# Optimization experiments

Measured on AMD Instinct MI355X. Metric: run time of the kernel, lower is better.

## Reference

```python
import jax, jax.numpy as jnp
import numpy as np

VOCAB = 50257
WORD_DIM = 300
HIDDEN = 256
BATCH = 256   # number of trees
LEAVES = 1024  # leaves per complete binary tree (power of 2)


def setup_inputs() -> dict:
    key = jax.random.key(0)
    k_ids, k_emb, k_w1, k_b1, k_w2, k_b2 = jax.random.split(key, 6)
    word_ids = jax.random.randint(k_ids, (BATCH, LEAVES), 0, VOCAB)
    emb_table = jax.random.normal(k_emb, (VOCAB, WORD_DIM), dtype=jnp.float32) * 0.1
    W1 = jax.random.normal(k_w1, (WORD_DIM, HIDDEN), dtype=jnp.float32) * (1.0 / np.sqrt(WORD_DIM))
    b1 = jax.random.normal(k_b1, (HIDDEN,), dtype=jnp.float32) * 0.01
    W2 = jax.random.normal(k_w2, (2 * HIDDEN, HIDDEN), dtype=jnp.float32) * (1.0 / np.sqrt(2 * HIDDEN))
    b2 = jax.random.normal(k_b2, (HIDDEN,), dtype=jnp.float32) * 0.01
    return {"word_ids": word_ids, "emb_table": emb_table, "W1": W1, "b1": b1, "W2": W2, "b2": b2}


def reference(word_ids, emb_table, W1, b1, W2, b2):
    # Leaves: embedding lookup + word2hidden linear (no nonlinearity, as in source)
    h = jnp.einsum('blw,wh->blh', emb_table[word_ids], W1) + b1  # [B, L, H]
    # Internal nodes: concat(left, right) @ W2 + b2, level by level up the
    # complete binary tree. Loop count = log2(LEAVES), a small static constant.
    while h.shape[1] > 1:
        B, n, H = h.shape
        pairs = h.reshape(B, n // 2, 2 * H)  # concat of sibling states
        h = jnp.einsum('bnk,kh->bnh', pairs, W2) + b2
    return h[:, 0, :]  # root hidden state per tree: [B, H]
```

## Files before the change

### kernel.cpp

```cpp
#include <hip/hip_runtime.h>
#include <hip/hip_bf16.h>
#include <stdint.h>

#define VOCAB 50257
#define WD 300
#define KP1 320
#define MP 50432

using bf16 = __hip_bfloat16;
typedef __attribute__((ext_vector_type(4))) float f32x4;
typedef __attribute__((ext_vector_type(8))) short bf16x8;

__device__ __forceinline__ void async_load16(const void* g, void* l) {
    __builtin_amdgcn_global_load_lds(
        (const __attribute__((address_space(1))) uint32_t*)(uintptr_t)g,
        (__attribute__((address_space(3))) uint32_t*)l, 16, 0, 0);
}

__global__ void prep_w(const float* __restrict__ W1, const float* __restrict__ W2,
                       const float* __restrict__ b2,
                       bf16* __restrict__ w1t, bf16* __restrict__ w2t,
                       bf16* __restrict__ w2b, float* __restrict__ b4,
                       float* __restrict__ zbuf) {
    if (blockIdx.x == 1344) {
        __shared__ float b2s[256];
        int n = threadIdx.x;
        b2s[n] = b2[n];
        zbuf[n] = 0.0f;
        __syncthreads();
        float acc = b2s[n];
        #pragma unroll 8
        for (int k = 0; k < 256; ++k)
            acc += b2s[k] * (W2[k * 256 + n] + W2[(k + 256) * 256 + n]);
        b4[n] = acc;
        return;
    }
    int idx = blockIdx.x * 256 + threadIdx.x;
    if (idx < 256 * KP1) {
        int n = idx / KP1;
        int k = idx - n * KP1;
        w1t[idx] = __float2bfloat16(k < WD ? W1[k * 256 + n] : 0.0f);
    } else if (idx < 256 * KP1 + 131072) {
        int j = idx - 256 * KP1;
        int n = j >> 9, k = j & 511;
        w2t[j] = __float2bfloat16(W2[k * 256 + n]);
    } else {
        int j = idx - 256 * KP1 - 131072;
        w2b[j] = __float2bfloat16(W2[j]);
    }
}

template <int AMODE, bool OUT_F32>
__device__ __forceinline__ void tile_gemm(
    char* smem, const void* Av, const int* ids,
    const bf16* BT, int Bstr, const float* bias,
    void* C, int Cs, int coff, int K, int As, int m0,
    const float* zbuf)
{
    constexpr int ASZ = (AMODE == 2) ? 16384 : 8192;
    constexpr int BSZ = 16384, STAGE = ASZ + BSZ;

    const int t = threadIdx.x, w = t >> 6, lane = t & 63;
    const int rg = w >> 2, cgr = w & 3, mi = lane & 15, q = lane >> 4;
    const bf16* Ab = (const bf16*)Av;

    int4 idq = {0, 0, 0, 0};
    if constexpr (AMODE == 1) idq = ((const int4*)ids)[m0 + (t >> 2)];

    auto stage = [&](int ke, int buf) {
        char* Asm = smem + buf * STAGE;
        char* Bsm = Asm + ASZ;
        if constexpr (AMODE == 2) {
            const float* A32 = (const float*)Av;
            #pragma unroll
            for (int i = 0; i < 2; ++i) {
                int s = i * 512 + t;
                int row = s >> 3;
                int kcd = (s & 7) ^ (row & 7);
                int k = ke + kcd * 4;
                int grow = m0 + row; if (grow >= VOCAB) grow = VOCAB - 1;
                const float* g = (k <= 296) ? (A32 + (size_t)grow * WD + k) : zbuf;
                async_load16(g, Asm + i * 8192 + w * 1024);
            }
        } else {
            int row = t >> 2;
            int kcd = (t & 3) ^ ((row >> 2) & 3);
            const bf16* g;
            if constexpr (AMODE == 1) {
                int sel = ke >> 8;
                int id = (sel & 2) ? ((sel & 1) ? idq.w : idq.z)
                                   : ((sel & 1) ? idq.y : idq.x);
                g = Ab + (size_t)id * 256 + (ke & 255) + kcd * 8;
            } else {
                g = Ab + (size_t)(m0 + row) * As + ke + kcd * 8;
            }
            async_load16(g, Asm + w * 1024);
        }
        #pragma unroll
        for (int i = 0; i < 2; ++i) {
            int s = i * 512 + t;
            int col = s >> 2;
            int kcd = (s & 3) ^ ((col >> 2) & 3);
            async_load16(BT + (size_t)col * Bstr + ke + kcd * 8,
                         Bsm + i * 8192 + w * 1024);
        }
    };

    f32x4 acc[4][4] = {};

    auto compute = [&](int buf) {
        const char* Asm = smem + buf * STAGE;
        const bf16* Bs16 = (const bf16*)(Asm + ASZ);
        bf16x8 af[4], bfr[4];
        if constexpr (AMODE == 2) {
            const float* As32 = (const float*)Asm;
            #pragma unroll
            for (int r = 0; r < 4; ++r) {
                int row = rg * 64 + r * 16 + mi;
                int sl = row * 8 + ((2 * q) ^ (row & 7));
                f32x4 lo = *(const f32x4*)(As32 + sl * 4);
                f32x4 hi = *(const f32x4*)(As32 + (sl ^ 1) * 4);
                union { bf16x8 v; bf16 hh[8]; } u;
                #pragma unroll
                for (int j = 0; j < 4; ++j) u.hh[j] = __float2bfloat16(lo[j]);
                #pragma unroll
                for (int j = 0; j < 4; ++j) u.hh[4 + j] = __float2bfloat16(hi[j]);
                af[r] = u.v;
            }
        } else {
            const bf16* As16 = (const bf16*)Asm;
            #pragma unroll
            for (int r = 0; r < 4; ++r) {
                int row = rg * 64 + r * 16 + mi;
                int slot = row * 4 + (q ^ ((row >> 2) & 3));
                af[r] = *(const bf16x8*)(As16 + slot * 8);
            }
        }
        #pragma unroll
        for (int c = 0; c < 4; ++c) {
            int col = cgr * 64 + c * 16 + mi;
            int slot = col * 4 + (q ^ ((col >> 2) & 3));
            bfr[c] = *(const bf16x8*)(Bs16 + slot * 8);
        }
        #pragma unroll
        for (int r = 0; r < 4; ++r)
            #pragma unroll
            for (int c = 0; c < 4; ++c)
                acc[r][c] = __builtin_amdgcn_mfma_f32_16x16x32_bf16(af[r], bfr[c], acc[r][c], 0, 0, 0);
    };

    const int S = K >> 5;
    if constexpr (AMODE == 2) {
        stage(0, 0);
        for (int k0 = 0; k0 < S; ++k0) {
            if (k0 + 1 < S) {
                stage((k0 + 1) * 32, (k0 + 1) & 1);
                asm volatile("s_waitcnt vmcnt(4)\n\ts_barrier" ::: "memory");
            } else {
                asm volatile("s_waitcnt vmcnt(0)\n\ts_barrier" ::: "memory");
            }
            compute(k0 & 1);
            asm volatile("s_waitcnt lgkmcnt(0)\n\ts_barrier" ::: "memory");
        }
    } else {
        stage(0, 0);
        if (S > 1) stage(32, 1);
        for (int k0 = 0; k0 < S; ++k0) {
            if (k0 + 1 < S)
                asm volatile("s_waitcnt vmcnt(3)\n\ts_barrier" ::: "memory");
            else
                asm volatile("s_waitcnt vmcnt(0)\n\ts_barrier" ::: "memory");
            if (k0 + 2 < S) stage((k0 + 2) * 32, (k0 + 2) % 3);
            compute(k0 % 3);
        }
    }

    #pragma unroll
    for (int r = 0; r < 4; ++r) {
        int rowb = m0 + rg * 64 + r * 16 + q * 4;
        #pragma unroll
        for (int c = 0; c < 4; ++c) {
            int col = cgr * 64 + c * 16 + mi;
            float bv = bias[col];
            #pragma unroll
            for (int i = 0; i < 4; ++i) {
                float v = acc[r][c][i] + bv;
                size_t o = (size_t)(rowb + i) * Cs + coff + col;
                if (OUT_F32) ((float*)C)[o] = v;
                else         ((bf16*)C)[o] = __float2bfloat16(v);
            }
        }
    }
}

__global__ __launch_bounds__(512)
void combo(const float* __restrict__ emb, const bf16* __restrict__ w1t,
           const float* __restrict__ b1, const bf16* __restrict__ w2t,
           const bf16* __restrict__ w2b, bf16* __restrict__ w4t,
           bf16* __restrict__ proj, const float* __restrict__ zbuf) {
    __shared__ char smem[73728];
    int blk = blockIdx.x;
    if (blk < 8) {
        int j = blk >> 1, s = blk & 1;
        tile_gemm<0, false>(smem, w2t + 256 * (j >> 1), nullptr,
                            w2b + 65536 * (j & 1), 256, zbuf,
                            w4t, 1024, 256 * j, 256, 512, s * 128, nullptr);
    } else {
        tile_gemm<2, false>(smem, emb, nullptr, w1t, KP1, b1,
                            proj, 256, 0, KP1, WD, (blk - 8) * 128, zbuf);
    }
}

__global__ __launch_bounds__(512)
void mainK(const bf16* __restrict__ proj, const int* __restrict__ ids,
           const bf16* __restrict__ w4t, bf16* __restrict__ w4c,
           const float* __restrict__ b4, bf16* __restrict__ h) {
    __shared__ char smem[73728];
    if (blockIdx.x >= 512) {
        const int tid = (blockIdx.x - 512) * 512 + threadIdx.x;
        #pragma unroll
        for (int i = 0; i < 8; ++i) {
            int u = i * 4096 + tid;
            int ln = u & 63, ks = (u >> 6) & 31, cg = u >> 11;
            int mi2 = ln & 15, q2 = ln >> 4;
            *(int4*)(w4c + (size_t)u * 8) =
                *(const int4*)(w4t + (size_t)(cg * 16 + mi2) * 1024 + ks * 32 + q2 * 8);
        }
        return;
    }
    tile_gemm<1, false>(smem, proj, ids, w4t, 1024, b4,
                        h, 256, 0, 1024, 256, blockIdx.x * 128, nullptr);
}

__global__ __launch_bounds__(512)
void treeK(const bf16* __restrict__ h, const bf16* __restrict__ w4t,
           const bf16* __restrict__ w4c, const float* __restrict__ b4,
           float* __restrict__ out) {
    constexpr int ASZ = 8192, BSZ = 32768, STAGE = ASZ + BSZ;
    __shared__ char smem[2 * STAGE];
    __shared__ bf16 Ht[64 * 256];
    __shared__ bf16 Ht2[16 * 256];
    __shared__ bf16 Ht3[4 * 256];

    const int t = threadIdx.x, w = t >> 6, lane = t & 63;
    const int mi = lane & 15, q = lane >> 4;
    const int b = blockIdx.x;

    {
        auto stage = [&](int r, int buf) {
            char* As = smem + buf * STAGE;
            char* Bs = As + ASZ;
            const int kb = r * 64;
            {
                int row = t >> 3, c = t & 7;
                async_load16(h + (size_t)(64 * b + row) * 1024 + kb + ((c ^ (row & 7)) << 3),
                             As + w * 1024);
            }
            #pragma unroll
            for (int sub = 0; sub < 2; ++sub)
                #pragma unroll
                for (int i = 0; i < 2; ++i) {
                    int s = i * 512 + t;
                    int col = s >> 2;
                    int kcd = (s & 3) ^ ((col >> 2) & 3);
                    async_load16(w4t + (size_t)col * 1024 + kb + sub * 32 + kcd * 8,
                                 Bs + sub * 16384 + i * 8192 + w * 1024);
                }
        };
        f32x4 acc[4][2] = {};
        stage(0, 0);
        for (int r = 0; r < 16; ++r) {
            if (r + 1 < 16) {
                stage(r + 1, (r + 1) & 1);
                asm volatile("s_waitcnt vmcnt(5)\n\ts_barrier" ::: "memory");
            } else {
                asm volatile("s_waitcnt vmcnt(0)\n\ts_barrier" ::: "memory");
            }
            const bf16* As16 = (const bf16*)(smem + (r & 1) * STAGE);
            const bf16* Bb   = (const bf16*)(smem + (r & 1) * STAGE + ASZ);
            #pragma unroll
            for (int kk = 0; kk < 2; ++kk) {
                bf16x8 af[4], bfr[2];
                #pragma unroll
                for (int ri = 0; ri < 4; ++ri) {
                    int row = ri * 16 + mi;
                    int c = kk * 4 + q;
                    af[ri] = *(const bf16x8*)(As16 + (row * 8 + (c ^ (row & 7))) * 8);
                }
                #pragma unroll
                for (int c4 = 0; c4 < 2; ++c4) {
                    int col = w * 32 + c4 * 16 + mi;
                    int slot = col * 4 + (q ^ ((col >> 2) & 3));
                    bfr[c4] = *(const bf16x8*)(Bb + kk * 8192 + slot * 8);
                }
                #pragma unroll
                for (int ri = 0; ri < 4; ++ri)
                    #pragma unroll
                    for (int c4 = 0; c4 < 2; ++c4)
                        acc[ri][c4] = __builtin_amdgcn_mfma_f32_16x16x32_bf16(af[ri], bfr[c4], acc[ri][c4], 0, 0, 0);
            }
            asm volatile("s_waitcnt lgkmcnt(0)\n\ts_barrier" ::: "memory");
        }
        #pragma unroll
        for (int ri = 0; ri < 4; ++ri) {
            #pragma unroll
            for (int c4 = 0; c4 < 2; ++c4) {
                int col = w * 32 + c4 * 16 + mi;
                float bv = b4[col];
                int chunk = col >> 3;
                #pragma unroll
                for (int i = 0; i < 4; ++i) {
                    int row = ri * 16 + q * 4 + i;
                    Ht[(row * 32 + (chunk ^ (row & 31))) * 8 + (col & 7)] =
                        __float2bfloat16(acc[ri][c4][i] + bv);
                }
            }
        }
    }
    __syncthreads();

    {
        f32x4 acc[2] = {};
        #pragma unroll 8
        for (int ks = 0; ks < 32; ++ks) {
            int kc = (ks & 7) * 4 + q;
            int r2 = 4 * mi + (ks >> 3);
            bf16x8 a = *(const bf16x8*)(Ht + (r2 * 32 + (kc ^ (r2 & 31))) * 8);
            #pragma unroll
            for (int g = 0; g < 2; ++g) {
                bf16x8 bb = *(const bf16x8*)(w4c + ((size_t)((2 * w + g) * 32 + ks) * 64 + lane) * 8);
                acc[g] = __builtin_amdgcn_mfma_f32_16x16x32_bf16(a, bb, acc[g], 0, 0, 0);
            }
        }
        #pragma unroll
        for (int g = 0; g < 2; ++g) {
            int col = w * 32 + g * 16 + mi;
            float bv = b4[col];
            int chunk = col >> 3;
            #pragma unroll
            for (int i = 0; i < 4; ++i) {
                int row = q * 4 + i;
                Ht2[(row * 32 + (chunk ^ (row & 15))) * 8 + (col & 7)] =
                    __float2bfloat16(acc[g][i] + bv);
            }
        }
    }
    __syncthreads();

    {
        f32x4 acc[2] = {};
        #pragma unroll 8
        for (int ks = 0; ks < 32; ++ks) {
            int kc = (ks & 7) * 4 + q;
            int r3 = (4 * mi + (ks >> 3)) & 15;
            bf16x8 a = *(const bf16x8*)(Ht2 + (r3 * 32 + (kc ^ (r3 & 15))) * 8);
            #pragma unroll
            for (int g = 0; g < 2; ++g) {
                bf16x8 bb = *(const bf16x8*)(w4c + ((size_t)((2 * w + g) * 32 + ks) * 64 + lane) * 8);
                acc[g] = __builtin_amdgcn_mfma_f32_16x16x32_bf16(a, bb, acc[g], 0, 0, 0);
            }
        }
        if (q == 0) {
            #pragma unroll
            for (int g = 0; g < 2; ++g) {
                int col = w * 32 + g * 16 + mi;
                float bv = b4[col];
                #pragma unroll
                for (int i = 0; i < 4; ++i)
                    Ht3[i * 256 + col] = __float2bfloat16(acc[g][i] + bv);
            }
        }
    }
    __syncthreads();

    {
        f32x4 acc[2] = {};
        #pragma unroll 8
        for (int ks = 0; ks < 32; ++ks) {
            int r4 = (4 * mi + (ks >> 3)) & 3;
            bf16x8 a = *(const bf16x8*)(Ht3 + r4 * 256 + (ks & 7) * 32 + q * 8);
            #pragma unroll
            for (int g = 0; g < 2; ++g) {
                bf16x8 bb = *(const bf16x8*)(w4c + ((size_t)((2 * w + g) * 32 + ks) * 64 + lane) * 8);
                acc[g] = __builtin_amdgcn_mfma_f32_16x16x32_bf16(a, bb, acc[g], 0, 0, 0);
            }
        }
        if (q == 0) {
            #pragma unroll
            for (int g = 0; g < 2; ++g) {
                int col = w * 32 + g * 16 + mi;
                out[(size_t)b * 256 + col] = acc[g][0] + b4[col];
            }
        }
    }
}

extern "C" void kernel_launch(void* const* d_in, const int* in_sizes, int n_in,
                              void* d_out, int out_size, void* d_ws, size_t ws_size,
                              hipStream_t stream) {
    const int*   ids = (const int*)d_in[0];
    const float* emb = (const float*)d_in[1];
    const float* W1  = (const float*)d_in[2];
    const float* b1  = (const float*)d_in[3];
    const float* W2  = (const float*)d_in[4];
    const float* b2  = (const float*)d_in[5];
    (void)in_sizes; (void)n_in; (void)out_size; (void)ws_size;

    char* ws = (char*)d_ws;
    size_t off = 0;
    float* zbuf = (float*)(ws + off); off += 1024;
    float* b4   = (float*)(ws + off); off += 1024;
    bf16* w1t = (bf16*)(ws + off); off += (size_t)256 * KP1 * 2;
    bf16* w2t = (bf16*)(ws + off); off += (size_t)256 * 512 * 2;
    bf16* w2b = (bf16*)(ws + off); off += (size_t)512 * 256 * 2;
    bf16* w4t = (bf16*)(ws + off); off += (size_t)256 * 1024 * 2;
    bf16* w4c = (bf16*)(ws + off); off += (size_t)256 * 1024 * 2;
    bf16* proj = (bf16*)(ws + off); off += (size_t)MP * 256 * 2;
    bf16* h  = (bf16*)(ws + off); off += (size_t)65536 * 256 * 2;
    (void)off;

    prep_w<<<1345, 256, 0, stream>>>(W1, W2, b2, w1t, w2t, w2b, b4, zbuf);

    combo<<<402, 512, 0, stream>>>(emb, w1t, b1, w2t, w2b, w4t, proj, zbuf);

    mainK<<<520, 512, 0, stream>>>(proj, ids, w4t, w4c, b4, h);

    treeK<<<256, 512, 0, stream>>>(h, w4t, w4c, b4, (float*)d_out);
}
```

Baseline: 200.1 us.

## Rewrite leaf-to-level GEMM with register-resident B fragments and narrower column tiles

The w4c reshuffle moves out of the main GEMM into its own small kernel. The main GEMM is rewritten so each block computes 128 rows by 128 columns (1024 blocks). B fragments are loaded directly from the pre-swizzled w4c into registers instead of going through LDS, and only the gathered A tiles are staged through a 4-deep LDS ring. This cuts LDS traffic and shared memory per block and doubles block count for occupancy, at the cost of an extra kernel launch and reading A twice (once per column half).

Result: slower. 223.0 us (+11.4%).

```diff
diff --git a/kernel.cpp b/kernel.cpp
--- a/kernel.cpp
+++ b/kernel.cpp
@@ -64,9 +64,6 @@
     const int rg = w >> 2, cgr = w & 3, mi = lane & 15, q = lane >> 4;
     const bf16* Ab = (const bf16*)Av;
 
-    int4 idq = {0, 0, 0, 0};
-    if constexpr (AMODE == 1) idq = ((const int4*)ids)[m0 + (t >> 2)];
-
     auto stage = [&](int ke, int buf) {
         char* Asm = smem + buf * STAGE;
         char* Bsm = Asm + ASZ;
@@ -85,15 +82,7 @@
         } else {
             int row = t >> 2;
             int kcd = (t & 3) ^ ((row >> 2) & 3);
-            const bf16* g;
-            if constexpr (AMODE == 1) {
-                int sel = ke >> 8;
-                int id = (sel & 2) ? ((sel & 1) ? idq.w : idq.z)
-                                   : ((sel & 1) ? idq.y : idq.x);
-                g = Ab + (size_t)id * 256 + (ke & 255) + kcd * 8;
-            } else {
-                g = Ab + (size_t)(m0 + row) * As + ke + kcd * 8;
-            }
+            const bf16* g = Ab + (size_t)(m0 + row) * As + ke + kcd * 8;
             async_load16(g, Asm + w * 1024);
         }
         #pragma unroll
@@ -191,6 +180,7 @@
             }
         }
     }
+    (void)ids;
 }
 
 __global__ __launch_bounds__(512)
@@ -212,24 +202,79 @@
 }
 
 __global__ __launch_bounds__(512)
+void w4cK(const bf16* __restrict__ w4t, bf16* __restrict__ w4c) {
+    const int tid = blockIdx.x * 512 + threadIdx.x;
+    #pragma unroll
+    for (int i = 0; i < 8; ++i) {
+        int u = i * 4096 + tid;
+        int ln = u & 63, ks = (u >> 6) & 31, cg = u >> 11;
+        int mi2 = ln & 15, q2 = ln >> 4;
+        *(int4*)(w4c + (size_t)u * 8) =
+            *(const int4*)(w4t + (size_t)(cg * 16 + mi2) * 1024 + ks * 32 + q2 * 8);
+    }
+}
+
+__global__ __launch_bounds__(512)
 void mainK(const bf16* __restrict__ proj, const int* __restrict__ ids,
-           const bf16* __restrict__ w4t, bf16* __restrict__ w4c,
-           const float* __restrict__ b4, bf16* __restrict__ h) {
-    __shared__ char smem[73728];
-    if (blockIdx.x >= 512) {
-        const int tid = (blockIdx.x - 512) * 512 + threadIdx.x;
-        #pragma unroll
-        for (int i = 0; i < 8; ++i) {
-            int u = i * 4096 + tid;
-            int ln = u & 63, ks = (u >> 6) & 31, cg = u >> 11;
-            int mi2 = ln & 15, q2 = ln >> 4;
-            *(int4*)(w4c + (size_t)u * 8) =
-                *(const int4*)(w4t + (size_t)(cg * 16 + mi2) * 1024 + ks * 32 + q2 * 8);
-        }
-        return;
-    }
-    tile_gemm<1, false>(smem, proj, ids, w4t, 1024, b4,
-                        h, 256, 0, 1024, 256, blockIdx.x * 128, nullptr);
+           const bf16* __restrict__ w4c, const float* __restrict__ b4,
+           bf16* __restrict__ h) {
+    __shared__ char Abuf[4][8192];
+    const int t = threadIdx.x, w = t >> 6, lane = t & 63;
+    const int mi = lane & 15, q = lane >> 4;
+    const int rt = blockIdx.x >> 1, ch = blockIdx.x & 1;
+    const int m0 = rt * 128;
+    const int c0 = ch * 128;
+    const int cg = ch * 8 + w;
+
+    const int4 idq = ((const int4*)ids)[m0 + (t >> 2)];
+
+    auto stageA = [&](int r, int buf) {
+        int ke = r * 32;
+        int row = t >> 2;
+        int kcd = (t & 3) ^ ((row >> 2) & 3);
+        int sel = ke >> 8;
+        int id = (sel & 2) ? ((sel & 1) ? idq.w : idq.z)
+                           : ((sel & 1) ? idq.y : idq.x);
+        async_load16(proj + (size_t)id * 256 + (ke & 255) + kcd * 8,
+                     Abuf[buf] + w * 1024);
+        (void)row;
+    };
+
+    f32x4 acc[8] = {};
+    bf16x8 bp[2];
+
+    stageA(0, 0); stageA(1, 1);
+    bp[0] = *(const bf16x8*)(w4c + ((size_t)(cg * 32 + 0) * 64 + lane) * 8);
+
+    #pragma unroll
+    for (int r = 0; r < 32; ++r) {
+        if (r + 2 < 32) stageA(r + 2, (r + 2) & 3);
+        if (r + 1 < 32)
+            bp[(r + 1) & 1] = *(const bf16x8*)(
+                w4c + ((size_t)(cg * 32 + (r + 1)) * 64 + lane) * 8);
+        if (r + 1 < 32)
+            asm volatile("s_waitcnt vmcnt(2) lgkmcnt(0)\n\ts_barrier" ::: "memory");
+        else
+            asm volatile("s_waitcnt vmcnt(0) lgkmcnt(0)\n\ts_barrier" ::: "memory");
+        const bf16* As16 = (const bf16*)Abuf[r & 3];
+        #pragma unroll
+        for (int ri = 0; ri < 8; ++ri) {
+            int row = ri * 16 + mi;
+            int slot = row * 4 + (q ^ ((row >> 2) & 3));
+            bf16x8 af = *(const bf16x8*)(As16 + slot * 8);
+            acc[ri] = __builtin_amdgcn_mfma_f32_16x16x32_bf16(af, bp[r & 1], acc[ri], 0, 0, 0);
+        }
+    }
+
+    const int col = c0 + w * 16 + mi;
+    const float bv = b4[col];
+    #pragma unroll
+    for (int ri = 0; ri < 8; ++ri) {
+        int rowb = m0 + ri * 16 + q * 4;
+        #pragma unroll
+        for (int i = 0; i < 4; ++i)
+            h[(size_t)(rowb + i) * 256 + col] = __float2bfloat16(acc[ri][i] + bv);
+    }
 }
 
 __global__ __launch_bounds__(512)
@@ -423,7 +468,9 @@
 
     combo<<<402, 512, 0, stream>>>(emb, w1t, b1, w2t, w2b, w4t, proj, zbuf);
 
-    mainK<<<520, 512, 0, stream>>>(proj, ids, w4t, w4c, b4, h);
+    w4cK<<<8, 512, 0, stream>>>(w4t, w4c);
+
+    mainK<<<1024, 512, 0, stream>>>(proj, ids, w4c, b4, h);
 
     treeK<<<256, 512, 0, stream>>>(h, w4t, w4c, b4, (float*)d_out);
 }
```
